# Kernel tuning notes

Measured on AMD Instinct MI355X. Metric: run time of the kernel, lower is better.

## Reference

```python
import jax, jax.numpy as jnp
import numpy as np

MIN_DURATION = 0.0
MAX_DURATION = 75.0
MAX_LEN = 80  # hard-coded output length from regulate_length's slice/pad to 80
LN_EPS = 1e-6


def _conv1d_same(x, w, b):
    # x: [B, T, Cin], w: [K, Cin, Cout] -> [B, T, Cout]
    y = jax.lax.conv_general_dilated(
        x, w, window_strides=(1,), padding='SAME',
        dimension_numbers=('NWC', 'WIO', 'NWC'))
    return y + b


def _layernorm(x, gamma, beta):
    mu = jnp.mean(x, axis=-1, keepdims=True)
    var = jnp.mean(jnp.square(x - mu), axis=-1, keepdims=True)
    return (x - mu) * jax.lax.rsqrt(var + LN_EPS) * gamma + beta


def setup_inputs() -> dict:
    key = jax.random.key(0)
    ks = jax.random.split(key, 5)
    B, T, D, F, K = 2048, 128, 256, 256, 3
    scale = 0.05
    return {
        'encoder_output': jax.random.normal(ks[0], (B, T, D), jnp.float32),
        'conv1_w': jax.random.normal(ks[1], (K, D, F), jnp.float32) * scale,
        'conv1_b': jnp.zeros((F,), jnp.float32),
        'conv2_w': jax.random.normal(ks[2], (K, F, F), jnp.float32) * scale,
        'conv2_b': jnp.zeros((F,), jnp.float32),
        'ln_gamma': jnp.ones((F,), jnp.float32),
        'ln_beta': jnp.zeros((F,), jnp.float32),
        'dense_w': jax.random.normal(ks[3], (F, 1), jnp.float32) * scale,
        'dense_b': jnp.full((1,), 2.0, jnp.float32),  # bias so rounded durations are nontrivial
    }


def reference(encoder_output, conv1_w, conv1_b, conv2_w, conv2_b,
              ln_gamma, ln_beta, dense_w, dense_b):
    # --- variance predictor (dropout = identity at inference) ---
    x = jax.nn.relu(_conv1d_same(encoder_output, conv1_w, conv1_b))
    x = _layernorm(x, ln_gamma, ln_beta)
    x = jax.nn.relu(_conv1d_same(x, conv2_w, conv2_b))
    x = _layernorm(x, ln_gamma, ln_beta)
    predicted_durations = x @ dense_w + dense_b  # [B, T, 1]

    # --- regulate_length, fully vectorized over batch ---
    dur = jnp.round(jnp.clip(predicted_durations, MIN_DURATION, MAX_DURATION))
    dur = dur[..., 0].astype(jnp.int32)                 # [B, T]
    cum = jnp.cumsum(dur, axis=1)                       # [B, T]
    pos = jnp.arange(MAX_LEN, dtype=jnp.int32)          # [80]
    # source index for each output frame: searchsorted(cum, pos, side='right')
    idx = jnp.sum(pos[None, :, None] >= cum[:, None, :], axis=-1)  # [B, 80]
    valid = pos[None, :] < cum[:, -1:]                  # [B, 80]
    T = encoder_output.shape[1]
    gathered = jnp.take_along_axis(
        encoder_output, jnp.clip(idx, 0, T - 1)[..., None], axis=1)  # [B, 80, D]
    regulated = jnp.where(valid[..., None], gathered, 0.0)
    return regulated
```

## Files before the change

### kernel.cpp

```cpp
#include <hip/hip_runtime.h>
#include <hip/hip_bf16.h>
#include <math.h>

#define TT 128
#define CC 256
#define MAXLEN 80
#define KSTEPS 24
#define SLOTS 68
#define NCH16 32

typedef __attribute__((ext_vector_type(8))) _Float16 half8v;
typedef __attribute__((ext_vector_type(2))) _Float16 half2v;
typedef __attribute__((ext_vector_type(4))) float f32x4;

#define MSCALE 4096.0f
#define MINV   (1.0f/4096.0f)

__device__ __forceinline__ int chunkidx(int slot, int c16) {
    return slot * NCH16 + (c16 ^ (slot & 7));
}

__device__ __forceinline__ void split2(float x0, float x1, half2v& h, half2v& m) {
    h = __builtin_bit_cast(half2v, __builtin_amdgcn_cvt_pkrtz(x0, x1));
    m.x = (_Float16)fmaf((float)h.x, -MSCALE, x0 * MSCALE);
    m.y = (_Float16)fmaf((float)h.y, -MSCALE, x1 * MSCALE);
}

__global__ void va_prep(const float* __restrict__ w1, const float* __restrict__ w2,
                        half8v* __restrict__ wsB)
{
    const int idx = blockIdx.x * 256 + threadIdx.x;
    const int lane = idx & 63;
    int q = idx >> 6;
    const int nfg = q & 15;   q >>= 4;
    const int plane = q & 1;  q >>= 1;
    const int kk2 = q & 7;    q >>= 3;
    const int tap = q % 3;
    const int cv  = q / 3;
    const float* w = cv ? w2 : w1;
    const int co  = nfg * 16 + (lane & 15);
    const int ci0 = kk2 * 32 + (lane >> 4) * 8;
    half8v out;
    #pragma unroll
    for (int j = 0; j < 8; ++j) {
        const float x = w[tap * (CC * CC) + (ci0 + j) * CC + co];
        const _Float16 h = (_Float16)x;
        if (plane == 0) out[j] = h;
        else            out[j] = (_Float16)((x - (float)h) * MSCALE);
    }
    wsB[idx] = out;
}

__global__ __launch_bounds__(256, 2)
void va_conv(const float* __restrict__ enc,
             const float* __restrict__ b1g, const float* __restrict__ b2g,
             const float* __restrict__ gg,  const float* __restrict__ bbg,
             const float* __restrict__ dwg, const float* __restrict__ dbg,
             const half8v* __restrict__ wsB,
             int* __restrict__ durG)
{
    __shared__ half8v P[2][SLOTS * NCH16];
    __shared__ float sumS[4][80];
    __shared__ float sumQ[4][80];
    __shared__ float muS[80];
    __shared__ float rsS[80];

    const int bb   = blockIdx.x;
    const int b    = bb >> 1;
    const int base = (bb & 1) << 6;
    const int tid  = threadIdx.x;
    const int wid  = tid >> 6;
    const int lane = tid & 63;
    const int l15  = lane & 15;
    const int lg   = lane >> 4;
    const int NGc  = wid * 64;

    const f32x4* encB4 = reinterpret_cast<const f32x4*>(enc) + (size_t)b * (TT * 64);

    for (int m2 = tid; m2 < SLOTS * NCH16; m2 += 256) {
        const int slot = m2 >> 5;
        const int c16  = m2 & 31;
        const int ra   = base + slot - 2;
        half8v h8, m8;
        if (ra >= 0 && ra < TT) {
            const f32x4* src = encB4 + ra * 64 + c16 * 2;
            const f32x4 v0 = src[0], v1 = src[1];
            half2v hp, mp;
            split2(v0.x, v0.y, hp, mp); h8[0]=hp.x; h8[1]=hp.y; m8[0]=mp.x; m8[1]=mp.y;
            split2(v0.z, v0.w, hp, mp); h8[2]=hp.x; h8[3]=hp.y; m8[2]=mp.x; m8[3]=mp.y;
            split2(v1.x, v1.y, hp, mp); h8[4]=hp.x; h8[5]=hp.y; m8[4]=mp.x; m8[5]=mp.y;
            split2(v1.z, v1.w, hp, mp); h8[6]=hp.x; h8[7]=hp.y; m8[6]=mp.x; m8[7]=mp.y;
        } else {
            #pragma unroll
            for (int j = 0; j < 8; ++j) { h8[j] = (_Float16)0.f; m8[j] = (_Float16)0.f; }
        }
        const int ci = chunkidx(slot, c16);
        P[0][ci] = h8;
        P[1][ci] = m8;
    }
    __syncthreads();

    float gv[4], bvv[4];
    #pragma unroll
    for (int nf = 0; nf < 4; ++nf) {
        gv[nf]  = gg[NGc + nf * 16 + l15];
        bvv[nf] = bbg[NGc + nf * 16 + l15];
    }

    f32x4 accH[5][4];
    f32x4 accM[5][4];

    {
        const int F1[5] = {-1, 15, 31, 47, 49};
        #pragma unroll
        for (int nf = 0; nf < 4; ++nf) {
            const float bz = b1g[NGc + nf * 16 + l15];
            const f32x4 b4 = {bz, bz, bz, bz};
            const f32x4 z4 = {0.f, 0.f, 0.f, 0.f};
            #pragma unroll
            for (int mf = 0; mf < 5; ++mf) { accH[mf][nf] = b4; accM[mf][nf] = z4; }
        }
        #pragma unroll 1
        for (int ks = 0; ks < KSTEPS; ++ks) {
            const int tap = ks >> 3, kk2 = ks & 7;
            half8v B[8];
            {
                const int fb = (tap * 8 + kk2) * 2;
                #pragma unroll
                for (int p = 0; p < 2; ++p)
                    #pragma unroll
                    for (int nf = 0; nf < 4; ++nf)
                        B[p * 4 + nf] = wsB[(size_t)((fb + p) * 16 + (wid * 4 + nf)) * 64 + lane];
            }
            #pragma unroll
            for (int mf = 0; mf < 5; ++mf) {
                const int slot = F1[mf] + l15 + tap + 1;
                const int ci = chunkidx(slot, kk2 * 4 + lg);
                const half8v Ah = P[0][ci];
                const half8v Am = P[1][ci];
                #pragma unroll
                for (int nf = 0; nf < 4; ++nf) {
                    accH[mf][nf] = __builtin_amdgcn_mfma_f32_16x16x32_f16(Ah, B[nf],     accH[mf][nf], 0, 0, 0);
                    accM[mf][nf] = __builtin_amdgcn_mfma_f32_16x16x32_f16(Ah, B[4 + nf], accM[mf][nf], 0, 0, 0);
                    accM[mf][nf] = __builtin_amdgcn_mfma_f32_16x16x32_f16(Am, B[nf],     accM[mf][nf], 0, 0, 0);
                }
            }
        }
        #pragma unroll
        for (int mf = 0; mf < 5; ++mf)
            #pragma unroll
            for (int nf = 0; nf < 4; ++nf) {
                f32x4 v;
                #pragma unroll
                for (int e = 0; e < 4; ++e)
                    v[e] = fmaxf(fmaf(accM[mf][nf][e], MINV, accH[mf][nf][e]), 0.f);
                accH[mf][nf] = v;
            }
        #pragma unroll
        for (int mf = 0; mf < 5; ++mf)
            #pragma unroll
            for (int r = 0; r < 4; ++r) {
                float s = (accH[mf][0][r] + accH[mf][1][r]) + (accH[mf][2][r] + accH[mf][3][r]);
                float q = accH[mf][0][r] * accH[mf][0][r];
                q = fmaf(accH[mf][1][r], accH[mf][1][r], q);
                q = fmaf(accH[mf][2][r], accH[mf][2][r], q);
                q = fmaf(accH[mf][3][r], accH[mf][3][r], q);
                #pragma unroll
                for (int o = 1; o < 16; o <<= 1) {
                    s += __shfl_xor(s, o, 64);
                    q += __shfl_xor(q, o, 64);
                }
                if (l15 == 0) {
                    const int idx = F1[mf] + lg * 4 + r + 1;
                    sumS[wid][idx] = s;
                    sumQ[wid][idx] = q;
                }
            }
        __syncthreads();
        if (tid < 66) {
            const float S = (sumS[0][tid] + sumS[1][tid]) + (sumS[2][tid] + sumS[3][tid]);
            const float Q = (sumQ[0][tid] + sumQ[1][tid]) + (sumQ[2][tid] + sumQ[3][tid]);
            const float mu = S * (1.f / 256.f);
            const float var = fmaf(-mu, mu, Q * (1.f / 256.f));
            muS[tid] = mu;
            rsS[tid] = 1.0f / sqrtf(var + 1e-6f);
        }
        __syncthreads();
        _Float16* Ph = (_Float16*)&P[0][0];
        _Float16* Pm = (_Float16*)&P[1][0];
        #pragma unroll
        for (int mf = 0; mf < 5; ++mf)
            #pragma unroll
            for (int r = 0; r < 4; ++r) {
                const int row = F1[mf] + lg * 4 + r;
                const float mu = muS[row + 1];
                const float rs = rsS[row + 1];
                const bool valid = (base + row >= 0) && (base + row < TT);
                #pragma unroll
                for (int nf = 0; nf < 4; ++nf) {
                    float v = (accH[mf][nf][r] - mu) * rs * gv[nf] + bvv[nf];
                    if (!valid) v = 0.f;
                    const int col = NGc + nf * 16 + l15;
                    const int off = chunkidx(row + 2, col >> 3) * 8 + (col & 7);
                    const _Float16 h = (_Float16)v;
                    Ph[off] = h;
                    Pm[off] = (_Float16)fmaf((float)h, -MSCALE, v * MSCALE);
                }
            }
    }
    __syncthreads();

    {
        #pragma unroll
        for (int nf = 0; nf < 4; ++nf) {
            const float bz = b2g[NGc + nf * 16 + l15];
            const f32x4 b4 = {bz, bz, bz, bz};
            const f32x4 z4 = {0.f, 0.f, 0.f, 0.f};
            #pragma unroll
            for (int mf = 0; mf < 4; ++mf) { accH[mf][nf] = b4; accM[mf][nf] = z4; }
        }
        half8v B0[8], B1[8];
        auto loadB = [&](half8v (&Bp)[8], int ks) {
            const int tap = ks >> 3, kk2 = ks & 7;
            const int fb = ((3 + tap) * 8 + kk2) * 2;
            #pragma unroll
            for (int p = 0; p < 2; ++p)
                #pragma unroll
                for (int nf = 0; nf < 4; ++nf)
                    Bp[p * 4 + nf] = wsB[(size_t)((fb + p) * 16 + (wid * 4 + nf)) * 64 + lane];
        };
        auto doK = [&](const half8v (&Bp)[8], int ks) {
            const int tap = ks >> 3, kk2 = ks & 7;
            #pragma unroll
            for (int mf = 0; mf < 4; ++mf) {
                const int slot = mf * 16 + l15 + tap + 1;
                const int ci = chunkidx(slot, kk2 * 4 + lg);
                const half8v Ah = P[0][ci];
                const half8v Am = P[1][ci];
                #pragma unroll
                for (int nf = 0; nf < 4; ++nf) {
                    accH[mf][nf] = __builtin_amdgcn_mfma_f32_16x16x32_f16(Ah, Bp[nf],     accH[mf][nf], 0, 0, 0);
                    accM[mf][nf] = __builtin_amdgcn_mfma_f32_16x16x32_f16(Ah, Bp[4 + nf], accM[mf][nf], 0, 0, 0);
                    accM[mf][nf] = __builtin_amdgcn_mfma_f32_16x16x32_f16(Am, Bp[nf],     accM[mf][nf], 0, 0, 0);
                }
            }
        };
        loadB(B0, 0);
        #pragma unroll 1
        for (int ks = 0; ks < KSTEPS; ks += 2) {
            loadB(B1, ks + 1);
            doK(B0, ks);
            if (ks + 2 < KSTEPS) loadB(B0, ks + 2);
            doK(B1, ks + 1);
        }
        #pragma unroll
        for (int mf = 0; mf < 4; ++mf)
            #pragma unroll
            for (int nf = 0; nf < 4; ++nf) {
                f32x4 v;
                #pragma unroll
                for (int e = 0; e < 4; ++e)
                    v[e] = fmaxf(fmaf(accM[mf][nf][e], MINV, accH[mf][nf][e]), 0.f);
                accH[mf][nf] = v;
            }
        #pragma unroll
        for (int mf = 0; mf < 4; ++mf)
            #pragma unroll
            for (int r = 0; r < 4; ++r) {
                float s = (accH[mf][0][r] + accH[mf][1][r]) + (accH[mf][2][r] + accH[mf][3][r]);
                float q = accH[mf][0][r] * accH[mf][0][r];
                q = fmaf(accH[mf][1][r], accH[mf][1][r], q);
                q = fmaf(accH[mf][2][r], accH[mf][2][r], q);
                q = fmaf(accH[mf][3][r], accH[mf][3][r], q);
                #pragma unroll
                for (int o = 1; o < 16; o <<= 1) {
                    s += __shfl_xor(s, o, 64);
                    q += __shfl_xor(q, o, 64);
                }
                if (l15 == 0) {
                    const int idx = mf * 16 + lg * 4 + r;
                    sumS[wid][idx] = s;
                    sumQ[wid][idx] = q;
                }
            }
        __syncthreads();
        if (tid < 64) {
            const float S = (sumS[0][tid] + sumS[1][tid]) + (sumS[2][tid] + sumS[3][tid]);
            const float Q = (sumQ[0][tid] + sumQ[1][tid]) + (sumQ[2][tid] + sumQ[3][tid]);
            const float mu = S * (1.f / 256.f);
            const float var = fmaf(-mu, mu, Q * (1.f / 256.f));
            muS[tid] = mu;
            rsS[tid] = 1.0f / sqrtf(var + 1e-6f);
        }
        __syncthreads();
        float dv[4];
        #pragma unroll
        for (int nf = 0; nf < 4; ++nf) dv[nf] = dwg[NGc + nf * 16 + l15];
        #pragma unroll
        for (int mf = 0; mf < 4; ++mf)
            #pragma unroll
            for (int r = 0; r < 4; ++r) {
                const int row = mf * 16 + lg * 4 + r;
                const float mu = muS[row];
                const float rs = rsS[row];
                float p = 0.f;
                #pragma unroll
                for (int nf = 0; nf < 4; ++nf) {
                    const float v = (accH[mf][nf][r] - mu) * rs * gv[nf] + bvv[nf];
                    p = fmaf(v, dv[nf], p);
                }
                #pragma unroll
                for (int o = 1; o < 16; o <<= 1) p += __shfl_xor(p, o, 64);
                if (l15 == 0) sumS[wid][row] = p;
            }
        __syncthreads();
        if (tid < 64) {
            const float pd = (sumS[0][tid] + sumS[1][tid]) + (sumS[2][tid] + sumS[3][tid]) + dbg[0];
            const float dcl = fminf(fmaxf(pd, 0.0f), 75.0f);
            durG[b * TT + base + tid] = (int)rintf(dcl);
        }
    }
}

__global__ __launch_bounds__(256)
void va_gather(const float* __restrict__ enc, const int* __restrict__ durG,
               float* __restrict__ outg)
{
    __shared__ int cumS[TT];
    __shared__ int wtotS[2];
    const int b    = blockIdx.x;
    const int tid  = threadIdx.x;
    const int wid  = tid >> 6;
    const int lane = tid & 63;

    int sv = 0;
    if (tid < TT) {
        sv = durG[b * TT + tid];
        #pragma unroll
        for (int o = 1; o < 64; o <<= 1) {
            const int u = __shfl_up(sv, o, 64);
            if (lane >= o) sv += u;
        }
        if (lane == 63) wtotS[tid >> 6] = sv;
    }
    __syncthreads();
    if (tid < TT) {
        if (tid >= 64) sv += wtotS[0];
        cumS[tid] = sv;
    }
    __syncthreads();

    const int total = cumS[TT - 1];
    const f32x4* encB4 = reinterpret_cast<const f32x4*>(enc) + (size_t)b * (TT * 64);
    f32x4* outB4 = reinterpret_cast<f32x4*>(outg) + (size_t)b * (MAXLEN * 64);
    for (int pp = 0; pp < 20; ++pp) {
        const int p = wid * 20 + pp;
        int lo = 0, hi = TT;
        while (lo < hi) {
            const int mid = (lo + hi) >> 1;
            if (cumS[mid] <= p) lo = mid + 1; else hi = mid;
        }
        f32x4 v = {0.f, 0.f, 0.f, 0.f};
        if (p < total) {
            const int src = (lo < TT) ? lo : (TT - 1);
            v = encB4[src * 64 + lane];
        }
        outB4[p * 64 + lane] = v;
    }
}

extern "C" void kernel_launch(void* const* d_in, const int* in_sizes, int n_in,
                              void* d_out, int out_size, void* d_ws, size_t ws_size,
                              hipStream_t stream) {
    const float* enc = (const float*)d_in[0];
    const float* w1  = (const float*)d_in[1];
    const float* b1  = (const float*)d_in[2];
    const float* w2  = (const float*)d_in[3];
    const float* b2  = (const float*)d_in[4];
    const float* gam = (const float*)d_in[5];
    const float* bet = (const float*)d_in[6];
    const float* dw  = (const float*)d_in[7];
    const float* db  = (const float*)d_in[8];
    float* out = (float*)d_out;
    half8v* wsB = (half8v*)d_ws;
    int* durG = (int*)((char*)d_ws + 98304u * 16u);

    const int B = in_sizes[0] / (TT * CC);
    hipLaunchKernelGGL(va_prep, dim3(384), dim3(256), 0, stream, w1, w2, wsB);
    hipLaunchKernelGGL(va_conv, dim3(B * 2), dim3(256), 0, stream,
                       enc, b1, b2, gam, bet, dw, db, wsB, durG);
    hipLaunchKernelGGL(va_gather, dim3(B), dim3(256), 0, stream, enc, durG, out);
}
```

Baseline: 633.2 us.

## Fuse length-regulation gather into conv kernel and prefetch conv1 weights

Drops the separate gather kernel. A per-batch atomic counter lets the second of the two conv blocks for each batch, once both have written their durations, compute the prefix sum and gather the output rows. Conv1 weight fragments are now double-buffered from global memory the way conv2 already was. Both MFMA loops are wrapped in s_setprio, and two barriers are removed by having each wave compute the LayerNorm statistics redundantly. This saves a launch and some latency, at the cost of a memset, atomics with thread fences, and more register pressure.

Measured after the change: 1.084 ms. 71.3% more time.

```diff
diff --git a/kernel.cpp b/kernel.cpp
--- a/kernel.cpp
+++ b/kernel.cpp
@@ -57,13 +57,18 @@
              const float* __restrict__ gg,  const float* __restrict__ bbg,
              const float* __restrict__ dwg, const float* __restrict__ dbg,
              const half8v* __restrict__ wsB,
-             int* __restrict__ durG)
+             int* __restrict__ durG, int* __restrict__ cntG,
+             float* __restrict__ outg)
 {
     __shared__ half8v P[2][SLOTS * NCH16];
     __shared__ float sumS[4][80];
     __shared__ float sumQ[4][80];
     __shared__ float muS[80];
     __shared__ float rsS[80];
+    __shared__ float dsum[4][64];
+    __shared__ int   cumS[TT];
+    __shared__ int   wtotS[2];
+    __shared__ int   flagS;
 
     const int bb   = blockIdx.x;
     const int b    = bb >> 1;
@@ -111,7 +116,6 @@
     f32x4 accM[5][4];
 
     {
-        const int F1[5] = {-1, 15, 31, 47, 49};
         #pragma unroll
         for (int nf = 0; nf < 4; ++nf) {
             const float bz = b1g[NGc + nf * 16 + l15];
@@ -120,31 +124,42 @@
             #pragma unroll
             for (int mf = 0; mf < 5; ++mf) { accH[mf][nf] = b4; accM[mf][nf] = z4; }
         }
-        #pragma unroll 1
-        for (int ks = 0; ks < KSTEPS; ++ks) {
+        half8v B0[8], B1[8];
+        auto loadB1 = [&](half8v (&Bp)[8], int ks) {
             const int tap = ks >> 3, kk2 = ks & 7;
-            half8v B[8];
-            {
-                const int fb = (tap * 8 + kk2) * 2;
-                #pragma unroll
-                for (int p = 0; p < 2; ++p)
-                    #pragma unroll
-                    for (int nf = 0; nf < 4; ++nf)
-                        B[p * 4 + nf] = wsB[(size_t)((fb + p) * 16 + (wid * 4 + nf)) * 64 + lane];
-            }
+            const int fb = (tap * 8 + kk2) * 2;
+            #pragma unroll
+            for (int p = 0; p < 2; ++p)
+                #pragma unroll
+                for (int nf = 0; nf < 4; ++nf)
+                    Bp[p * 4 + nf] = wsB[(size_t)((fb + p) * 16 + (wid * 4 + nf)) * 64 + lane];
+        };
+        auto doK1 = [&](const half8v (&Bp)[8], int ks) {
+            const int tap = ks >> 3, kk2 = ks & 7;
             #pragma unroll
             for (int mf = 0; mf < 5; ++mf) {
+                constexpr int F1[5] = {-1, 15, 31, 47, 49};
                 const int slot = F1[mf] + l15 + tap + 1;
                 const int ci = chunkidx(slot, kk2 * 4 + lg);
                 const half8v Ah = P[0][ci];
                 const half8v Am = P[1][ci];
+                __builtin_amdgcn_s_setprio(1);
                 #pragma unroll
                 for (int nf = 0; nf < 4; ++nf) {
-                    accH[mf][nf] = __builtin_amdgcn_mfma_f32_16x16x32_f16(Ah, B[nf],     accH[mf][nf], 0, 0, 0);
-                    accM[mf][nf] = __builtin_amdgcn_mfma_f32_16x16x32_f16(Ah, B[4 + nf], accM[mf][nf], 0, 0, 0);
-                    accM[mf][nf] = __builtin_amdgcn_mfma_f32_16x16x32_f16(Am, B[nf],     accM[mf][nf], 0, 0, 0);
-                }
-            }
+                    accH[mf][nf] = __builtin_amdgcn_mfma_f32_16x16x32_f16(Ah, Bp[nf],     accH[mf][nf], 0, 0, 0);
+                    accM[mf][nf] = __builtin_amdgcn_mfma_f32_16x16x32_f16(Ah, Bp[4 + nf], accM[mf][nf], 0, 0, 0);
+                    accM[mf][nf] = __builtin_amdgcn_mfma_f32_16x16x32_f16(Am, Bp[nf],     accM[mf][nf], 0, 0, 0);
+                }
+                __builtin_amdgcn_s_setprio(0);
+            }
+        };
+        loadB1(B0, 0);
+        #pragma unroll 1
+        for (int ks = 0; ks < KSTEPS; ks += 2) {
+            loadB1(B1, ks + 1);
+            doK1(B0, ks);
+            if (ks + 2 < KSTEPS) loadB1(B0, ks + 2);
+            doK1(B1, ks + 1);
         }
         #pragma unroll
         for (int mf = 0; mf < 5; ++mf)
@@ -156,6 +171,7 @@
                     v[e] = fmaxf(fmaf(accM[mf][nf][e], MINV, accH[mf][nf][e]), 0.f);
                 accH[mf][nf] = v;
             }
+        constexpr int F1c[5] = {-1, 15, 31, 47, 49};
         #pragma unroll
         for (int mf = 0; mf < 5; ++mf)
             #pragma unroll
@@ -171,28 +187,27 @@
                     q += __shfl_xor(q, o, 64);
                 }
                 if (l15 == 0) {
-                    const int idx = F1[mf] + lg * 4 + r + 1;
+                    const int idx = F1c[mf] + lg * 4 + r + 1;
                     sumS[wid][idx] = s;
                     sumQ[wid][idx] = q;
                 }
             }
         __syncthreads();
-        if (tid < 66) {
-            const float S = (sumS[0][tid] + sumS[1][tid]) + (sumS[2][tid] + sumS[3][tid]);
-            const float Q = (sumQ[0][tid] + sumQ[1][tid]) + (sumQ[2][tid] + sumQ[3][tid]);
+        for (int i = lane; i < 66; i += 64) {
+            const float S = (sumS[0][i] + sumS[1][i]) + (sumS[2][i] + sumS[3][i]);
+            const float Q = (sumQ[0][i] + sumQ[1][i]) + (sumQ[2][i] + sumQ[3][i]);
             const float mu = S * (1.f / 256.f);
             const float var = fmaf(-mu, mu, Q * (1.f / 256.f));
-            muS[tid] = mu;
-            rsS[tid] = 1.0f / sqrtf(var + 1e-6f);
-        }
-        __syncthreads();
+            muS[i] = mu;
+            rsS[i] = 1.0f / sqrtf(var + 1e-6f);
+        }
         _Float16* Ph = (_Float16*)&P[0][0];
         _Float16* Pm = (_Float16*)&P[1][0];
         #pragma unroll
         for (int mf = 0; mf < 5; ++mf)
             #pragma unroll
             for (int r = 0; r < 4; ++r) {
-                const int row = F1[mf] + lg * 4 + r;
+                const int row = F1c[mf] + lg * 4 + r;
                 const float mu = muS[row + 1];
                 const float rs = rsS[row + 1];
                 const bool valid = (base + row >= 0) && (base + row < TT);
@@ -237,12 +252,14 @@
                 const int ci = chunkidx(slot, kk2 * 4 + lg);
                 const half8v Ah = P[0][ci];
                 const half8v Am = P[1][ci];
+                __builtin_amdgcn_s_setprio(1);
                 #pragma unroll
                 for (int nf = 0; nf < 4; ++nf) {
                     accH[mf][nf] = __builtin_amdgcn_mfma_f32_16x16x32_f16(Ah, Bp[nf],     accH[mf][nf], 0, 0, 0);
                     accM[mf][nf] = __builtin_amdgcn_mfma_f32_16x16x32_f16(Ah, Bp[4 + nf], accM[mf][nf], 0, 0, 0);
                     accM[mf][nf] = __builtin_amdgcn_mfma_f32_16x16x32_f16(Am, Bp[nf],     accM[mf][nf], 0, 0, 0);
                 }
+                __builtin_amdgcn_s_setprio(0);
             }
         };
         loadB(B0, 0);
@@ -284,15 +301,15 @@
                 }
             }
         __syncthreads();
-        if (tid < 64) {
-            const float S = (sumS[0][tid] + sumS[1][tid]) + (sumS[2][tid] + sumS[3][tid]);
-            const float Q = (sumQ[0][tid] + sumQ[1][tid]) + (sumQ[2][tid] + sumQ[3][tid]);
+        if (lane < 64) {
+            const int i = lane;
+            const float S = (sumS[0][i] + sumS[1][i]) + (sumS[2][i] + sumS[3][i]);
+            const float Q = (sumQ[0][i] + sumQ[1][i]) + (sumQ[2][i] + sumQ[3][i]);
             const float mu = S * (1.f / 256.f);
             const float var = fmaf(-mu, mu, Q * (1.f / 256.f));
-            muS[tid] = mu;
-            rsS[tid] = 1.0f / sqrtf(var + 1e-6f);
-        }
-        __syncthreads();
+            muS[i] = mu;
+            rsS[i] = 1.0f / sqrtf(var + 1e-6f);
+        }
         float dv[4];
         #pragma unroll
         for (int nf = 0; nf < 4; ++nf) dv[nf] = dwg[NGc + nf * 16 + l15];
@@ -311,27 +328,24 @@
                 }
                 #pragma unroll
                 for (int o = 1; o < 16; o <<= 1) p += __shfl_xor(p, o, 64);
-                if (l15 == 0) sumS[wid][row] = p;
+                if (l15 == 0) dsum[wid][row] = p;
             }
         __syncthreads();
         if (tid < 64) {
-            const float pd = (sumS[0][tid] + sumS[1][tid]) + (sumS[2][tid] + sumS[3][tid]) + dbg[0];
+            const float pd = (dsum[0][tid] + dsum[1][tid]) + (dsum[2][tid] + dsum[3][tid]) + dbg[0];
             const float dcl = fminf(fmaxf(pd, 0.0f), 75.0f);
             durG[b * TT + base + tid] = (int)rintf(dcl);
         }
     }
-}
-
-__global__ __launch_bounds__(256)
-void va_gather(const float* __restrict__ enc, const int* __restrict__ durG,
-               float* __restrict__ outg)
-{
-    __shared__ int cumS[TT];
-    __shared__ int wtotS[2];
-    const int b    = blockIdx.x;
-    const int tid  = threadIdx.x;
-    const int wid  = tid >> 6;
-    const int lane = tid & 63;
+
+    __syncthreads();
+    if (tid == 0) {
+        __threadfence();
+        flagS = atomicAdd(&cntG[b], 1);
+    }
+    __syncthreads();
+    if (flagS != 1) return;
+    __threadfence();
 
     int sv = 0;
     if (tid < TT) {
@@ -351,7 +365,6 @@
     __syncthreads();
 
     const int total = cumS[TT - 1];
-    const f32x4* encB4 = reinterpret_cast<const f32x4*>(enc) + (size_t)b * (TT * 64);
     f32x4* outB4 = reinterpret_cast<f32x4*>(outg) + (size_t)b * (MAXLEN * 64);
     for (int pp = 0; pp < 20; ++pp) {
         const int p = wid * 20 + pp;
@@ -382,12 +395,14 @@
     const float* dw  = (const float*)d_in[7];
     const float* db  = (const float*)d_in[8];
     float* out = (float*)d_out;
+
+    const int B = in_sizes[0] / (TT * CC);
     half8v* wsB = (half8v*)d_ws;
     int* durG = (int*)((char*)d_ws + 98304u * 16u);
-
-    const int B = in_sizes[0] / (TT * CC);
+    int* cntG = (int*)((char*)d_ws + 98304u * 16u + (size_t)B * TT * 4);
+
+    hipMemsetAsync(cntG, 0, B * sizeof(int), stream);
     hipLaunchKernelGGL(va_prep, dim3(384), dim3(256), 0, stream, w1, w2, wsB);
     hipLaunchKernelGGL(va_conv, dim3(B * 2), dim3(256), 0, stream,
-                       enc, b1, b2, gam, bet, dw, db, wsB, durG);
-    hipLaunchKernelGGL(va_gather, dim3(B), dim3(256), 0, stream, enc, durG, out);
+                       enc, b1, b2, gam, bet, dw, db, wsB, durG, cntG, out);
 }
```

## Split each sequence into four 32-row conv tiles with higher occupancy

Applied to the files above, without the earlier changes.

The fused conv kernel now processes 32 output rows per block instead of 64, so it launches four blocks per batch element. It cuts LDS and accumulator usage so three blocks fit per CU instead of two. The barrier before the layernorm stats are consumed is removed by having every wave compute the per-row mean and rstd redundantly. Conv2's double-buffered weight prefetch is replaced by a simple per-step load. In exchange, halo rows are recomputed for a larger share of the conv1 tile, and each weight fragment is read by twice as many blocks.

Measured after the change: 736.2 us. +16.3%, slower.

```diff
diff --git a/kernel.cpp b/kernel.cpp
--- a/kernel.cpp
+++ b/kernel.cpp
@@ -6,7 +6,7 @@
 #define CC 256
 #define MAXLEN 80
 #define KSTEPS 24
-#define SLOTS 68
+#define SLOTS 36
 #define NCH16 32
 
 typedef __attribute__((ext_vector_type(8))) _Float16 half8v;
@@ -51,7 +51,7 @@
     wsB[idx] = out;
 }
 
-__global__ __launch_bounds__(256, 2)
+__global__ __launch_bounds__(256, 3)
 void va_conv(const float* __restrict__ enc,
              const float* __restrict__ b1g, const float* __restrict__ b2g,
              const float* __restrict__ gg,  const float* __restrict__ bbg,
@@ -60,14 +60,15 @@
              int* __restrict__ durG)
 {
     __shared__ half8v P[2][SLOTS * NCH16];
-    __shared__ float sumS[4][80];
-    __shared__ float sumQ[4][80];
-    __shared__ float muS[80];
-    __shared__ float rsS[80];
+    __shared__ float sumS[4][40];
+    __shared__ float sumQ[4][40];
+    __shared__ float muS[40];
+    __shared__ float rsS[40];
+    __shared__ float dsum[4][32];
 
     const int bb   = blockIdx.x;
-    const int b    = bb >> 1;
-    const int base = (bb & 1) << 6;
+    const int b    = bb >> 2;
+    const int base = (bb & 3) << 5;
     const int tid  = threadIdx.x;
     const int wid  = tid >> 6;
     const int lane = tid & 63;
@@ -107,18 +108,17 @@
         bvv[nf] = bbg[NGc + nf * 16 + l15];
     }
 
-    f32x4 accH[5][4];
-    f32x4 accM[5][4];
+    f32x4 accH[3][4];
+    f32x4 accM[3][4];
 
     {
-        const int F1[5] = {-1, 15, 31, 47, 49};
         #pragma unroll
         for (int nf = 0; nf < 4; ++nf) {
             const float bz = b1g[NGc + nf * 16 + l15];
             const f32x4 b4 = {bz, bz, bz, bz};
             const f32x4 z4 = {0.f, 0.f, 0.f, 0.f};
             #pragma unroll
-            for (int mf = 0; mf < 5; ++mf) { accH[mf][nf] = b4; accM[mf][nf] = z4; }
+            for (int mf = 0; mf < 3; ++mf) { accH[mf][nf] = b4; accM[mf][nf] = z4; }
         }
         #pragma unroll 1
         for (int ks = 0; ks < KSTEPS; ++ks) {
@@ -133,7 +133,8 @@
                         B[p * 4 + nf] = wsB[(size_t)((fb + p) * 16 + (wid * 4 + nf)) * 64 + lane];
             }
             #pragma unroll
-            for (int mf = 0; mf < 5; ++mf) {
+            for (int mf = 0; mf < 3; ++mf) {
+                constexpr int F1[3] = {-1, 15, 17};
                 const int slot = F1[mf] + l15 + tap + 1;
                 const int ci = chunkidx(slot, kk2 * 4 + lg);
                 const half8v Ah = P[0][ci];
@@ -147,7 +148,7 @@
             }
         }
         #pragma unroll
-        for (int mf = 0; mf < 5; ++mf)
+        for (int mf = 0; mf < 3; ++mf)
             #pragma unroll
             for (int nf = 0; nf < 4; ++nf) {
                 f32x4 v;
@@ -156,8 +157,9 @@
                     v[e] = fmaxf(fmaf(accM[mf][nf][e], MINV, accH[mf][nf][e]), 0.f);
                 accH[mf][nf] = v;
             }
-        #pragma unroll
-        for (int mf = 0; mf < 5; ++mf)
+        constexpr int F1c[3] = {-1, 15, 17};
+        #pragma unroll
+        for (int mf = 0; mf < 3; ++mf)
             #pragma unroll
             for (int r = 0; r < 4; ++r) {
                 float s = (accH[mf][0][r] + accH[mf][1][r]) + (accH[mf][2][r] + accH[mf][3][r]);
@@ -171,28 +173,28 @@
                     q += __shfl_xor(q, o, 64);
                 }
                 if (l15 == 0) {
-                    const int idx = F1[mf] + lg * 4 + r + 1;
+                    const int idx = F1c[mf] + lg * 4 + r + 1;
                     sumS[wid][idx] = s;
                     sumQ[wid][idx] = q;
                 }
             }
         __syncthreads();
-        if (tid < 66) {
-            const float S = (sumS[0][tid] + sumS[1][tid]) + (sumS[2][tid] + sumS[3][tid]);
-            const float Q = (sumQ[0][tid] + sumQ[1][tid]) + (sumQ[2][tid] + sumQ[3][tid]);
+        if (lane < 34) {
+            const int i = lane;
+            const float S = (sumS[0][i] + sumS[1][i]) + (sumS[2][i] + sumS[3][i]);
+            const float Q = (sumQ[0][i] + sumQ[1][i]) + (sumQ[2][i] + sumQ[3][i]);
             const float mu = S * (1.f / 256.f);
             const float var = fmaf(-mu, mu, Q * (1.f / 256.f));
-            muS[tid] = mu;
-            rsS[tid] = 1.0f / sqrtf(var + 1e-6f);
-        }
-        __syncthreads();
+            muS[i] = mu;
+            rsS[i] = 1.0f / sqrtf(var + 1e-6f);
+        }
         _Float16* Ph = (_Float16*)&P[0][0];
         _Float16* Pm = (_Float16*)&P[1][0];
         #pragma unroll
-        for (int mf = 0; mf < 5; ++mf)
+        for (int mf = 0; mf < 3; ++mf)
             #pragma unroll
             for (int r = 0; r < 4; ++r) {
-                const int row = F1[mf] + lg * 4 + r;
+                const int row = F1c[mf] + lg * 4 + r;
                 const float mu = muS[row + 1];
                 const float rs = rsS[row + 1];
                 const bool valid = (base + row >= 0) && (base + row < TT);
@@ -217,44 +219,36 @@
             const f32x4 b4 = {bz, bz, bz, bz};
             const f32x4 z4 = {0.f, 0.f, 0.f, 0.f};
             #pragma unroll
-            for (int mf = 0; mf < 4; ++mf) { accH[mf][nf] = b4; accM[mf][nf] = z4; }
-        }
-        half8v B0[8], B1[8];
-        auto loadB = [&](half8v (&Bp)[8], int ks) {
+            for (int mf = 0; mf < 2; ++mf) { accH[mf][nf] = b4; accM[mf][nf] = z4; }
+        }
+        #pragma unroll 1
+        for (int ks = 0; ks < KSTEPS; ++ks) {
             const int tap = ks >> 3, kk2 = ks & 7;
-            const int fb = ((3 + tap) * 8 + kk2) * 2;
-            #pragma unroll
-            for (int p = 0; p < 2; ++p)
-                #pragma unroll
-                for (int nf = 0; nf < 4; ++nf)
-                    Bp[p * 4 + nf] = wsB[(size_t)((fb + p) * 16 + (wid * 4 + nf)) * 64 + lane];
-        };
-        auto doK = [&](const half8v (&Bp)[8], int ks) {
-            const int tap = ks >> 3, kk2 = ks & 7;
-            #pragma unroll
-            for (int mf = 0; mf < 4; ++mf) {
+            half8v B[8];
+            {
+                const int fb = ((3 + tap) * 8 + kk2) * 2;
+                #pragma unroll
+                for (int p = 0; p < 2; ++p)
+                    #pragma unroll
+                    for (int nf = 0; nf < 4; ++nf)
+                        B[p * 4 + nf] = wsB[(size_t)((fb + p) * 16 + (wid * 4 + nf)) * 64 + lane];
+            }
+            #pragma unroll
+            for (int mf = 0; mf < 2; ++mf) {
                 const int slot = mf * 16 + l15 + tap + 1;
                 const int ci = chunkidx(slot, kk2 * 4 + lg);
                 const half8v Ah = P[0][ci];
                 const half8v Am = P[1][ci];
                 #pragma unroll
                 for (int nf = 0; nf < 4; ++nf) {
-                    accH[mf][nf] = __builtin_amdgcn_mfma_f32_16x16x32_f16(Ah, Bp[nf],     accH[mf][nf], 0, 0, 0);
-                    accM[mf][nf] = __builtin_amdgcn_mfma_f32_16x16x32_f16(Ah, Bp[4 + nf], accM[mf][nf], 0, 0, 0);
-                    accM[mf][nf] = __builtin_amdgcn_mfma_f32_16x16x32_f16(Am, Bp[nf],     accM[mf][nf], 0, 0, 0);
-                }
-            }
-        };
-        loadB(B0, 0);
-        #pragma unroll 1
-        for (int ks = 0; ks < KSTEPS; ks += 2) {
-            loadB(B1, ks + 1);
-            doK(B0, ks);
-            if (ks + 2 < KSTEPS) loadB(B0, ks + 2);
-            doK(B1, ks + 1);
-        }
-        #pragma unroll
-        for (int mf = 0; mf < 4; ++mf)
+                    accH[mf][nf] = __builtin_amdgcn_mfma_f32_16x16x32_f16(Ah, B[nf],     accH[mf][nf], 0, 0, 0);
+                    accM[mf][nf] = __builtin_amdgcn_mfma_f32_16x16x32_f16(Ah, B[4 + nf], accM[mf][nf], 0, 0, 0);
+                    accM[mf][nf] = __builtin_amdgcn_mfma_f32_16x16x32_f16(Am, B[nf],     accM[mf][nf], 0, 0, 0);
+                }
+            }
+        }
+        #pragma unroll
+        for (int mf = 0; mf < 2; ++mf)
             #pragma unroll
             for (int nf = 0; nf < 4; ++nf) {
                 f32x4 v;
@@ -264,7 +258,7 @@
                 accH[mf][nf] = v;
             }
         #pragma unroll
-        for (int mf = 0; mf < 4; ++mf)
+        for (int mf = 0; mf < 2; ++mf)
             #pragma unroll
             for (int r = 0; r < 4; ++r) {
                 float s = (accH[mf][0][r] + accH[mf][1][r]) + (accH[mf][2][r] + accH[mf][3][r]);
@@ -284,20 +278,20 @@
                 }
             }
         __syncthreads();
-        if (tid < 64) {
-            const float S = (sumS[0][tid] + sumS[1][tid]) + (sumS[2][tid] + sumS[3][tid]);
-            const float Q = (sumQ[0][tid] + sumQ[1][tid]) + (sumQ[2][tid] + sumQ[3][tid]);
+        if (lane < 32) {
+            const int i = lane;
+            const float S = (sumS[0][i] + sumS[1][i]) + (sumS[2][i] + sumS[3][i]);
+            const float Q = (sumQ[0][i] + sumQ[1][i]) + (sumQ[2][i] + sumQ[3][i]);
             const float mu = S * (1.f / 256.f);
             const float var = fmaf(-mu, mu, Q * (1.f / 256.f));
-            muS[tid] = mu;
-            rsS[tid] = 1.0f / sqrtf(var + 1e-6f);
-        }
-        __syncthreads();
+            muS[i] = mu;
+            rsS[i] = 1.0f / sqrtf(var + 1e-6f);
+        }
         float dv[4];
         #pragma unroll
         for (int nf = 0; nf < 4; ++nf) dv[nf] = dwg[NGc + nf * 16 + l15];
         #pragma unroll
-        for (int mf = 0; mf < 4; ++mf)
+        for (int mf = 0; mf < 2; ++mf)
             #pragma unroll
             for (int r = 0; r < 4; ++r) {
                 const int row = mf * 16 + lg * 4 + r;
@@ -311,11 +305,11 @@
                 }
                 #pragma unroll
                 for (int o = 1; o < 16; o <<= 1) p += __shfl_xor(p, o, 64);
-                if (l15 == 0) sumS[wid][row] = p;
+                if (l15 == 0) dsum[wid][row] = p;
             }
         __syncthreads();
-        if (tid < 64) {
-            const float pd = (sumS[0][tid] + sumS[1][tid]) + (sumS[2][tid] + sumS[3][tid]) + dbg[0];
+        if (tid < 32) {
+            const float pd = (dsum[0][tid] + dsum[1][tid]) + (dsum[2][tid] + dsum[3][tid]) + dbg[0];
             const float dcl = fminf(fmaxf(pd, 0.0f), 75.0f);
             durG[b * TT + base + tid] = (int)rintf(dcl);
         }
@@ -382,12 +376,13 @@
     const float* dw  = (const float*)d_in[7];
     const float* db  = (const float*)d_in[8];
     float* out = (float*)d_out;
+
+    const int B = in_sizes[0] / (TT * CC);
     half8v* wsB = (half8v*)d_ws;
     int* durG = (int*)((char*)d_ws + 98304u * 16u);
 
-    const int B = in_sizes[0] / (TT * CC);
     hipLaunchKernelGGL(va_prep, dim3(384), dim3(256), 0, stream, w1, w2, wsB);
-    hipLaunchKernelGGL(va_conv, dim3(B * 2), dim3(256), 0, stream,
+    hipLaunchKernelGGL(va_conv, dim3(B * 4), dim3(256), 0, stream,
                        enc, b1, b2, gam, bet, dw, db, wsB, durG);
     hipLaunchKernelGGL(va_gather, dim3(B), dim3(256), 0, stream, enc, durG, out);
 }
```
